# Performance work log

Hardware: AMD Instinct MI355X
Metric: run time of the kernel (lower is better)

The kernel has to match this reference:

```python
import jax, jax.numpy as jnp
import numpy as np

B, S, D, H = 4, 2048, 1024, 16
HD = D // H


def setup_inputs() -> dict:
    key = jax.random.key(0)
    ks = jax.random.split(key, 12)
    inp = {
        "query": jax.random.normal(ks[0], (B, S, D), jnp.float32),
        "key": jax.random.normal(ks[1], (B, S, D), jnp.float32),
        "value": jax.random.normal(ks[2], (B, S, D), jnp.float32),
        "mask": jnp.tril(jnp.ones((S, S), jnp.int32)),  # causal mask
        "Wq": jax.random.normal(ks[3], (D, D), jnp.float32) / np.sqrt(D),
        "bq": jax.random.normal(ks[4], (D,), jnp.float32) * 0.02,
        "Wk": jax.random.normal(ks[5], (D, D), jnp.float32) / np.sqrt(D),
        "bk": jax.random.normal(ks[6], (D,), jnp.float32) * 0.02,
        "Wv": jax.random.normal(ks[7], (D, D), jnp.float32) / np.sqrt(D),
        "bv": jax.random.normal(ks[8], (D,), jnp.float32) * 0.02,
        "Wo": jax.random.normal(ks[9], (D, D), jnp.float32) / np.sqrt(D),
        "bo": jax.random.normal(ks[10], (D,), jnp.float32) * 0.02,
    }
    return inp


def reference(query, key, value, mask, Wq, bq, Wk, bk, Wv, bv, Wo, bo):
    # Linear projections (torch nn.Linear: y = x @ W.T + b)
    q = query @ Wq.T + bq
    k = key @ Wk.T + bk
    v = value @ Wv.T + bv
    # split heads: [B, S, D] -> [B, H, S, HD]
    q = q.reshape(B, S, H, HD).transpose(0, 2, 1, 3)
    k = k.reshape(B, S, H, HD).transpose(0, 2, 1, 3)
    v = v.reshape(B, S, H, HD).transpose(0, 2, 1, 3)
    # scaled dot-product attention with full [B,H,S,S] scores (faithful to source)
    scores = jnp.einsum("bhqd,bhkd->bhqk", q, k) / jnp.sqrt(jnp.float32(HD))
    scores = jnp.where(mask == 0, -jnp.inf, scores)
    attn = jax.nn.softmax(scores, axis=-1)
    out = jnp.einsum("bhqk,bhkd->bhqd", attn, v)
    # merge heads and output projection (dropout rate = 0.0 -> identity)
    out = out.transpose(0, 2, 1, 3).reshape(B, S, D)
    return out @ Wo.T + bo
```

## Files before the change

### kernel.cpp

```cpp
#include <hip/hip_runtime.h>

typedef __bf16 bf16x8 __attribute__((ext_vector_type(8)));
typedef float f32x4 __attribute__((ext_vector_type(4)));
typedef float f32x16 __attribute__((ext_vector_type(16)));
typedef unsigned short ushort;

__device__ __forceinline__ int4 cvt8(float4 a, float4 b) {
  bf16x8 v;
  v[0] = (__bf16)a.x; v[1] = (__bf16)a.y; v[2] = (__bf16)a.z; v[3] = (__bf16)a.w;
  v[4] = (__bf16)b.x; v[5] = (__bf16)b.y; v[6] = (__bf16)b.z; v[7] = (__bf16)b.w;
  return __builtin_bit_cast(int4, v);
}

__device__ __forceinline__ void gld16(const void* g, void* l) {
  __builtin_amdgcn_global_load_lds(
      (const __attribute__((address_space(1))) void*)g,
      (__attribute__((address_space(3))) void*)l, 16, 0, 0);
}

__device__ __forceinline__ unsigned pkbf(float a, float b) {
  const unsigned x = __builtin_bit_cast(ushort, (__bf16)a);
  const unsigned y = __builtin_bit_cast(ushort, (__bf16)b);
  return x | (y << 16);
}

#if __has_builtin(__builtin_amdgcn_permlane32_swap)
typedef unsigned u32x2 __attribute__((ext_vector_type(2)));
__device__ __forceinline__ void plswap(unsigned& a, unsigned& b, int hi) {
  (void)hi;
  u32x2 r = __builtin_amdgcn_permlane32_swap(a, b, false, false);
  a = r[0]; b = r[1];
}
#else
__device__ __forceinline__ void plswap(unsigned& a, unsigned& b, int hi) {
  const unsigned pa = (unsigned)__shfl_xor((int)a, 32);
  const unsigned pb = (unsigned)__shfl_xor((int)b, 32);
  const unsigned x = hi ? pb : a;
  const unsigned y = hi ? b : pa;
  a = x; b = y;
}
#endif

__device__ __forceinline__ f32x16 mfma32(bf16x8 a, bf16x8 b, f32x16 c) {
  return __builtin_amdgcn_mfma_f32_32x32x16_bf16(a, b, c, 0, 0, 0);
}

__global__ __launch_bounds__(256) void cvt4_k(const float* __restrict__ i0,
                                              const float* __restrict__ i1,
                                              const float* __restrict__ i2,
                                              const float* __restrict__ i3,
                                              ushort* __restrict__ o, int n8) {
  const int z = blockIdx.y;
  const float* in = (z == 0) ? i0 : (z == 1) ? i1 : (z == 2) ? i2 : i3;
  ushort* out = o + (size_t)z * 1024 * 1024;
  int i = blockIdx.x * 256 + threadIdx.x;
  if (i >= n8) return;
  const float4* p = (const float4*)in + (size_t)i * 2;
  *(int4*)(out + (size_t)i * 8) = cvt8(p[0], p[1]);
}

template <int AMODE, int WMODE, int OMODE>
__global__ __launch_bounds__(256) void gemm_k(const void* __restrict__ A,
                                              const void* __restrict__ W,
                                              const float* __restrict__ bias,
                                              void* __restrict__ Out,
                                              float oscale) {
  constexpr int K = 1024;
  __shared__ __align__(16) char lA[128 * 128];
  __shared__ __align__(16) char lB[128 * 128];
  const int t = threadIdx.x;
  const int l = t & 63;
  const int w = t >> 6;
  const int wr = w >> 1, wc = w & 1;
  const int m0 = blockIdx.x * 128;
  const int n0 = blockIdx.y * 128;
  const int srow = l >> 3;
  const int scol = ((l & 7) ^ srow) << 3;
  f32x4 acc[4][4];
#pragma unroll
  for (int i = 0; i < 4; ++i)
#pragma unroll
    for (int j = 0; j < 4; ++j) acc[i][j] = (f32x4){0.f, 0.f, 0.f, 0.f};

  for (int k0 = 0; k0 < K; k0 += 64) {
    if constexpr (AMODE == 1) {
#pragma unroll
      for (int i = 0; i < 4; ++i) {
        const int chunk = w * 4 + i;
        gld16((const ushort*)A + (size_t)(m0 + chunk * 8 + srow) * K + k0 + scol,
              lA + chunk * 1024);
      }
    } else {
#pragma unroll
      for (int qq = 0; qq < 4; ++qq) {
        const int L = t * 8 + qq * 2048;
        const int r = L >> 6, c = L & 63;
        const int dst = r * 128 + ((c * 2) ^ ((r & 7) << 4));
        const float* s0 = (const float*)A + (size_t)(m0 + r) * K + k0 + c;
        *(int4*)(lA + dst) = cvt8(*(const float4*)s0, *(const float4*)(s0 + 4));
      }
    }
    if constexpr (WMODE == 1) {
#pragma unroll
      for (int i = 0; i < 4; ++i) {
        const int chunk = w * 4 + i;
        gld16((const ushort*)W + (size_t)(n0 + chunk * 8 + srow) * K + k0 + scol,
              lB + chunk * 1024);
      }
    } else {
#pragma unroll
      for (int qq = 0; qq < 4; ++qq) {
        const int L = t * 8 + qq * 2048;
        const int r = L >> 6, c = L & 63;
        const int dst = r * 128 + ((c * 2) ^ ((r & 7) << 4));
        const float* s1 = (const float*)W + (size_t)(n0 + r) * K + k0 + c;
        *(int4*)(lB + dst) = cvt8(*(const float4*)s1, *(const float4*)(s1 + 4));
      }
    }
    __syncthreads();
#pragma unroll
    for (int ks = 0; ks < 2; ++ks) {
      const int kb = ks * 64 + ((l >> 4) << 4);
      bf16x8 af[4], bfv[4];
#pragma unroll
      for (int i = 0; i < 4; ++i) {
        const int row = wr * 64 + i * 16 + (l & 15);
        af[i] = *(const bf16x8*)(lA + row * 128 + (kb ^ ((row & 7) << 4)));
      }
#pragma unroll
      for (int j = 0; j < 4; ++j) {
        const int row = wc * 64 + j * 16 + (l & 15);
        bfv[j] = *(const bf16x8*)(lB + row * 128 + (kb ^ ((row & 7) << 4)));
      }
#pragma unroll
      for (int i = 0; i < 4; ++i)
#pragma unroll
        for (int j = 0; j < 4; ++j)
          acc[i][j] = __builtin_amdgcn_mfma_f32_16x16x32_bf16(af[i], bfv[j],
                                                              acc[i][j], 0, 0, 0);
    }
    __syncthreads();
  }
#pragma unroll
  for (int i = 0; i < 4; ++i)
#pragma unroll
    for (int j = 0; j < 4; ++j)
#pragma unroll
      for (int rg = 0; rg < 4; ++rg) {
        const int gm = m0 + wr * 64 + i * 16 + ((l >> 4) << 2) + rg;
        const int gn = n0 + wc * 64 + j * 16 + (l & 15);
        const float v = (acc[i][j][rg] + bias[gn]) * oscale;
        if constexpr (OMODE == 0) {
          const int b = gm >> 11, s = gm & 2047, h = gn >> 6, hd = gn & 63;
          ((ushort*)Out)[((((size_t)(b * 16 + h)) * 2048 + s) << 6) + hd] =
              __builtin_bit_cast(ushort, (__bf16)v);
        } else if constexpr (OMODE == 1) {
          const int b = gm >> 11, s = gm & 2047, h = gn >> 6, hd = gn & 63;
          ((ushort*)Out)[((((size_t)(b * 16 + h)) << 6) + hd) * 2048 + s] =
              __builtin_bit_cast(ushort, (__bf16)v);
        } else {
          ((float*)Out)[(size_t)gm * 1024 + gn] = v;
        }
      }
}

__global__ __launch_bounds__(256) void attn_k(const ushort* __restrict__ qh,
                                              const ushort* __restrict__ kh,
                                              const ushort* __restrict__ vth,
                                              ushort* __restrict__ out) {
  const int bh = blockIdx.x;
  const int t = threadIdx.x, l = t & 63, wv = t >> 6;
  const int lq = l & 31, hi = l >> 5;
  __shared__ __align__(16) char lk[2][64 * 128];
  __shared__ __align__(16) char lv[2][64 * 128];

  const int r0 = t >> 3;
  const int c0 = (t & 7) * 8;
  const ushort* kbase = kh + (size_t)bh * 2048 * 64 + (size_t)r0 * 64 + c0;
  const ushort* vbase = vth + (size_t)bh * 64 * 2048 + (size_t)r0 * 2048 + c0;
  const int dst0 = r0 * 128 + ((c0 * 2) ^ ((r0 & 7) << 4));
  const int b = bh >> 4, h = bh & 15;

  int4 ka, kb2, va, vb2;
#define LOAD_TILE(kv0)                                            \
  do {                                                            \
    ka  = *(const int4*)(kbase + (size_t)(kv0) * 64);             \
    kb2 = *(const int4*)(kbase + (size_t)(kv0) * 64 + 32 * 64);   \
    va  = *(const int4*)(vbase + (kv0));                          \
    vb2 = *(const int4*)(vbase + (kv0) + 32 * 2048);              \
  } while (0)
#define WRITE_TILE(buf)                                           \
  do {                                                            \
    *(int4*)(lk[buf] + dst0) = ka;                                \
    *(int4*)(lk[buf] + dst0 + 32 * 128) = kb2;                    \
    *(int4*)(lv[buf] + dst0) = va;                                \
    *(int4*)(lv[buf] + dst0 + 32 * 128) = vb2;                    \
  } while (0)

#pragma unroll 1
  for (int pass = 0; pass < 2; ++pass) {
    const int qt = pass ? (15 - blockIdx.y) : blockIdx.y;
    const int q0 = qt * 128;
    const int qrow = q0 + wv * 32 + lq;

    bf16x8 qf0, qf1, qf2, qf3;
    {
      const ushort* qp = qh + ((size_t)bh * 2048 + qrow) * 64 + hi * 8;
      qf0 = *(const bf16x8*)(qp);
      qf1 = *(const bf16x8*)(qp + 16);
      qf2 = *(const bf16x8*)(qp + 32);
      qf3 = *(const bf16x8*)(qp + 48);
    }
    LOAD_TILE(0);
    __syncthreads();
    WRITE_TILE(0);

    float m_r = -1e30f, l_r = 0.f;
    f32x16 acco[2];
#pragma unroll
    for (int dt = 0; dt < 2; ++dt)
#pragma unroll
      for (int r = 0; r < 16; ++r) acco[dt][r] = 0.f;

    const int nt = 2 * qt + 2;
    int cur = 0;
#pragma unroll 1
    for (int ti = 0; ti < nt; ++ti) {
      __syncthreads();
      if (ti + 1 < nt) LOAD_TILE((ti + 1) << 6);

#pragma unroll
      for (int s = 0; s < 2; ++s) {
        const int kvs = (ti << 6) + s * 32;
        if (kvs > q0 + wv * 32 + 31) continue;

        f32x16 p;
#pragma unroll
        for (int r = 0; r < 16; ++r) p[r] = 0.f;
        __builtin_amdgcn_s_setprio(1);
#pragma unroll
        for (int kd = 0; kd < 4; ++kd) {
          const int row = s * 32 + lq;
          const bf16x8 kf = *(const bf16x8*)(
              lk[cur] + row * 128 + ((kd * 32 + hi * 16) ^ ((row & 7) << 4)));
          const bf16x8 qf = (kd == 0) ? qf0 : (kd == 1) ? qf1 : (kd == 2) ? qf2 : qf3;
          p = mfma32(kf, qf, p);
        }
        __builtin_amdgcn_s_setprio(0);
        if (kvs + 31 > q0 + wv * 32) {
#pragma unroll
          for (int r = 0; r < 16; ++r) {
            const int kv = kvs + (r & 3) + 8 * (r >> 2) + 4 * hi;
            if (kv > qrow) p[r] = -1e30f;
          }
        }
        float red[8];
#pragma unroll
        for (int r = 0; r < 8; ++r) red[r] = fmaxf(p[r], p[r + 8]);
#pragma unroll
        for (int r = 0; r < 4; ++r) red[r] = fmaxf(red[r], red[r + 4]);
        float tm = fmaxf(fmaxf(red[0], red[1]), fmaxf(red[2], red[3]));
        tm = fmaxf(tm, __shfl_xor(tm, 32));
        if (!__all(tm <= m_r + 8.f)) {
          const float mn = fmaxf(m_r, tm);
          const float e = __builtin_amdgcn_exp2f(m_r - mn);
          m_r = mn;
          l_r *= e;
#pragma unroll
          for (int dt = 0; dt < 2; ++dt)
#pragma unroll
            for (int r = 0; r < 16; ++r) acco[dt][r] *= e;
        }
#pragma unroll
        for (int r = 0; r < 16; ++r) p[r] = __builtin_amdgcn_exp2f(p[r] - m_r);
        float sr[8];
#pragma unroll
        for (int r = 0; r < 8; ++r) sr[r] = p[r] + p[r + 8];
#pragma unroll
        for (int r = 0; r < 4; ++r) sr[r] = sr[r] + sr[r + 4];
        float rs = (sr[0] + sr[1]) + (sr[2] + sr[3]);
        rs += __shfl_xor(rs, 32);
        l_r += rs;
        unsigned W0a = pkbf(p[0], p[1]),   W0b = pkbf(p[2], p[3]);
        unsigned W1a = pkbf(p[4], p[5]),   W1b = pkbf(p[6], p[7]);
        unsigned W2a = pkbf(p[8], p[9]),   W2b = pkbf(p[10], p[11]);
        unsigned W3a = pkbf(p[12], p[13]), W3b = pkbf(p[14], p[15]);
#pragma unroll
        for (int ks = 0; ks < 2; ++ks) {
          unsigned a0 = ks ? W2a : W0a;
          unsigned a1 = ks ? W2b : W0b;
          unsigned b0 = ks ? W3a : W1a;
          unsigned b1 = ks ? W3b : W1b;
          plswap(a0, b0, hi);
          plswap(a1, b1, hi);
          const uint4 pw = {a0, a1, b0, b1};
          const bf16x8 pf = __builtin_bit_cast(bf16x8, pw);
          __builtin_amdgcn_s_setprio(1);
#pragma unroll
          for (int dt = 0; dt < 2; ++dt) {
            const int row = dt * 32 + lq;
            const bf16x8 vf = *(const bf16x8*)(
                lv[cur] + row * 128 +
                ((s * 64 + ks * 32 + hi * 16) ^ ((row & 7) << 4)));
            acco[dt] = mfma32(vf, pf, acco[dt]);
          }
          __builtin_amdgcn_s_setprio(0);
        }
      }
      if (ti + 1 < nt) WRITE_TILE(cur ^ 1);
      cur ^= 1;
    }
    const float inv = __builtin_amdgcn_rcpf(l_r);
    ushort* orow = out + ((size_t)(b * 2048 + qrow)) * 1024 + h * 64;
#pragma unroll
    for (int dt = 0; dt < 2; ++dt)
#pragma unroll
      for (int g = 0; g < 4; ++g) {
        ushort4 st;
        st.x = __builtin_bit_cast(ushort, (__bf16)(acco[dt][4 * g + 0] * inv));
        st.y = __builtin_bit_cast(ushort, (__bf16)(acco[dt][4 * g + 1] * inv));
        st.z = __builtin_bit_cast(ushort, (__bf16)(acco[dt][4 * g + 2] * inv));
        st.w = __builtin_bit_cast(ushort, (__bf16)(acco[dt][4 * g + 3] * inv));
        *(ushort4*)(orow + dt * 32 + g * 8 + hi * 4) = st;
      }
  }
#undef LOAD_TILE
#undef WRITE_TILE
}

extern "C" void kernel_launch(void* const* d_in, const int* in_sizes, int n_in,
                              void* d_out, int out_size, void* d_ws, size_t ws_size,
                              hipStream_t stream) {
  (void)in_sizes; (void)n_in; (void)out_size;
  const float* query = (const float*)d_in[0];
  const float* key = (const float*)d_in[1];
  const float* value = (const float*)d_in[2];
  const float* Wq = (const float*)d_in[4];
  const float* bq = (const float*)d_in[5];
  const float* Wk = (const float*)d_in[6];
  const float* bk = (const float*)d_in[7];
  const float* Wv = (const float*)d_in[8];
  const float* bv = (const float*)d_in[9];
  const float* Wo = (const float*)d_in[10];
  const float* bo = (const float*)d_in[11];

  char* ws = (char*)d_ws;
  const size_t SZA = (size_t)8192 * 1024 * 2;
  const size_t SZW = (size_t)1024 * 1024 * 2;
  ushort* qh = (ushort*)(ws + 0 * SZA);
  ushort* kh = (ushort*)(ws + 1 * SZA);
  ushort* vt = (ushort*)(ws + 2 * SZA);
  ushort* ao = (ushort*)(ws + 3 * SZA);
  dim3 bb(256), gg(64, 8), ga(64, 8);
  const float QS = 0.125f * 1.44269504088896f;

  if (ws_size >= 4 * SZA + 4 * SZW) {
    ushort* wq = (ushort*)(ws + 4 * SZA);
    ushort* wk = (ushort*)(ws + 4 * SZA + 1 * SZW);
    ushort* wv = (ushort*)(ws + 4 * SZA + 2 * SZW);
    ushort* wo = (ushort*)(ws + 4 * SZA + 3 * SZW);
    const int n8w = 1024 * 1024 / 8;
    hipLaunchKernelGGL(cvt4_k, dim3(n8w / 256, 4), bb, 0, stream, Wq, Wk, Wv, Wo, wq, n8w);
    hipLaunchKernelGGL((gemm_k<0, 1, 0>), gg, bb, 0, stream, (const void*)query, (const void*)wq, bq, (void*)qh, QS);
    hipLaunchKernelGGL((gemm_k<0, 1, 0>), gg, bb, 0, stream, (const void*)key, (const void*)wk, bk, (void*)kh, 1.0f);
    hipLaunchKernelGGL((gemm_k<0, 1, 1>), gg, bb, 0, stream, (const void*)value, (const void*)wv, bv, (void*)vt, 1.0f);
    hipLaunchKernelGGL(attn_k, ga, bb, 0, stream, qh, kh, vt, ao);
    hipLaunchKernelGGL((gemm_k<1, 1, 2>), gg, bb, 0, stream, (const void*)ao, (const void*)wo, bo, d_out, 1.0f);
  } else {
    hipLaunchKernelGGL((gemm_k<0, 0, 0>), gg, bb, 0, stream, (const void*)query, (const void*)Wq, bq, (void*)qh, QS);
    hipLaunchKernelGGL((gemm_k<0, 0, 0>), gg, bb, 0, stream, (const void*)key, (const void*)Wk, bk, (void*)kh, 1.0f);
    hipLaunchKernelGGL((gemm_k<0, 0, 1>), gg, bb, 0, stream, (const void*)value, (const void*)Wv, bv, (void*)vt, 1.0f);
    hipLaunchKernelGGL(attn_k, ga, bb, 0, stream, qh, kh, vt, ao);
    hipLaunchKernelGGL((gemm_k<1, 0, 2>), gg, bb, 0, stream, (const void*)ao, (const void*)Wo, bo, d_out, 1.0f);
  }
}
```

Baseline: 206.8 us.

## Split paired causal query tiles into separate blocks and compute row sums via MFMA

The attention kernel stops processing two complementary query tiles per block. It launches one block per query tile, with twice as many blocks in y, ordered heaviest-first. The softmax row sum is now accumulated with an extra MFMA against a ones vector instead of VALU adds plus a cross-lane shuffle. The change also drops the s_setprio hints, reshapes the max reduction tree, and packs bf16 through a vector cast. This is meant to raise occupancy and parallelism and to cut VALU work, at the cost of losing the paired load balance and adding MFMA work and registers for the sum accumulator.

```diff
diff --git a/kernel.cpp b/kernel.cpp
--- a/kernel.cpp
+++ b/kernel.cpp
@@ -1,6 +1,7 @@
 #include <hip/hip_runtime.h>
 
 typedef __bf16 bf16x8 __attribute__((ext_vector_type(8)));
+typedef __bf16 bf16x2 __attribute__((ext_vector_type(2)));
 typedef float f32x4 __attribute__((ext_vector_type(4)));
 typedef float f32x16 __attribute__((ext_vector_type(16)));
 typedef unsigned short ushort;
@@ -19,9 +20,10 @@
 }
 
 __device__ __forceinline__ unsigned pkbf(float a, float b) {
-  const unsigned x = __builtin_bit_cast(ushort, (__bf16)a);
-  const unsigned y = __builtin_bit_cast(ushort, (__bf16)b);
-  return x | (y << 16);
+  bf16x2 v;
+  v[0] = (__bf16)a;
+  v[1] = (__bf16)b;
+  return __builtin_bit_cast(unsigned, v);
 }
 
 #if __has_builtin(__builtin_amdgcn_permlane32_swap)
@@ -169,17 +171,31 @@
                                               const ushort* __restrict__ vth,
                                               ushort* __restrict__ out) {
   const int bh = blockIdx.x;
+  const int qt = gridDim.y - 1 - blockIdx.y;
+  const int q0 = qt * 128;
   const int t = threadIdx.x, l = t & 63, wv = t >> 6;
   const int lq = l & 31, hi = l >> 5;
   __shared__ __align__(16) char lk[2][64 * 128];
   __shared__ __align__(16) char lv[2][64 * 128];
+
+  const int qrow = q0 + wv * 32 + lq;
+  bf16x8 qf0, qf1, qf2, qf3;
+  {
+    const ushort* qp = qh + ((size_t)bh * 2048 + qrow) * 64 + hi * 8;
+    qf0 = *(const bf16x8*)(qp);
+    qf1 = *(const bf16x8*)(qp + 16);
+    qf2 = *(const bf16x8*)(qp + 32);
+    qf3 = *(const bf16x8*)(qp + 48);
+  }
+  bf16x8 ones8;
+#pragma unroll
+  for (int i = 0; i < 8; ++i) ones8[i] = (__bf16)1.0f;
 
   const int r0 = t >> 3;
   const int c0 = (t & 7) * 8;
   const ushort* kbase = kh + (size_t)bh * 2048 * 64 + (size_t)r0 * 64 + c0;
   const ushort* vbase = vth + (size_t)bh * 64 * 2048 + (size_t)r0 * 2048 + c0;
   const int dst0 = r0 * 128 + ((c0 * 2) ^ ((r0 & 7) << 4));
-  const int b = bh >> 4, h = bh & 15;
 
   int4 ka, kb2, va, vb2;
 #define LOAD_TILE(kv0)                                            \
@@ -197,135 +213,115 @@
     *(int4*)(lv[buf] + dst0 + 32 * 128) = vb2;                    \
   } while (0)
 
+  LOAD_TILE(0);
+  WRITE_TILE(0);
+
+  float m_r = -1e30f;
+  f32x16 acco[2];
+  f32x16 acc_l;
+#pragma unroll
+  for (int dt = 0; dt < 2; ++dt)
+#pragma unroll
+    for (int r = 0; r < 16; ++r) acco[dt][r] = 0.f;
+#pragma unroll
+  for (int r = 0; r < 16; ++r) acc_l[r] = 0.f;
+
+  const int nt = 2 * qt + 2;
+  int cur = 0;
 #pragma unroll 1
-  for (int pass = 0; pass < 2; ++pass) {
-    const int qt = pass ? (15 - blockIdx.y) : blockIdx.y;
-    const int q0 = qt * 128;
-    const int qrow = q0 + wv * 32 + lq;
-
-    bf16x8 qf0, qf1, qf2, qf3;
-    {
-      const ushort* qp = qh + ((size_t)bh * 2048 + qrow) * 64 + hi * 8;
-      qf0 = *(const bf16x8*)(qp);
-      qf1 = *(const bf16x8*)(qp + 16);
-      qf2 = *(const bf16x8*)(qp + 32);
-      qf3 = *(const bf16x8*)(qp + 48);
-    }
-    LOAD_TILE(0);
+  for (int ti = 0; ti < nt; ++ti) {
     __syncthreads();
-    WRITE_TILE(0);
-
-    float m_r = -1e30f, l_r = 0.f;
-    f32x16 acco[2];
-#pragma unroll
-    for (int dt = 0; dt < 2; ++dt)
-#pragma unroll
-      for (int r = 0; r < 16; ++r) acco[dt][r] = 0.f;
-
-    const int nt = 2 * qt + 2;
-    int cur = 0;
-#pragma unroll 1
-    for (int ti = 0; ti < nt; ++ti) {
-      __syncthreads();
-      if (ti + 1 < nt) LOAD_TILE((ti + 1) << 6);
-
-#pragma unroll
-      for (int s = 0; s < 2; ++s) {
-        const int kvs = (ti << 6) + s * 32;
-        if (kvs > q0 + wv * 32 + 31) continue;
-
-        f32x16 p;
-#pragma unroll
-        for (int r = 0; r < 16; ++r) p[r] = 0.f;
-        __builtin_amdgcn_s_setprio(1);
-#pragma unroll
-        for (int kd = 0; kd < 4; ++kd) {
-          const int row = s * 32 + lq;
-          const bf16x8 kf = *(const bf16x8*)(
-              lk[cur] + row * 128 + ((kd * 32 + hi * 16) ^ ((row & 7) << 4)));
-          const bf16x8 qf = (kd == 0) ? qf0 : (kd == 1) ? qf1 : (kd == 2) ? qf2 : qf3;
-          p = mfma32(kf, qf, p);
+    if (ti + 1 < nt) LOAD_TILE((ti + 1) << 6);
+
+#pragma unroll
+    for (int s = 0; s < 2; ++s) {
+      const int kvs = (ti << 6) + s * 32;
+      if (kvs > q0 + wv * 32 + 31) continue;
+
+      f32x16 p;
+#pragma unroll
+      for (int r = 0; r < 16; ++r) p[r] = 0.f;
+#pragma unroll
+      for (int kd = 0; kd < 4; ++kd) {
+        const int row = s * 32 + lq;
+        const bf16x8 kf = *(const bf16x8*)(
+            lk[cur] + row * 128 + ((kd * 32 + hi * 16) ^ ((row & 7) << 4)));
+        const bf16x8 qf = (kd == 0) ? qf0 : (kd == 1) ? qf1 : (kd == 2) ? qf2 : qf3;
+        p = mfma32(kf, qf, p);
+      }
+      if (kvs + 31 > q0 + wv * 32) {
+#pragma unroll
+        for (int r = 0; r < 16; ++r) {
+          const int kv = kvs + (r & 3) + 8 * (r >> 2) + 4 * hi;
+          if (kv > qrow) p[r] = -1e30f;
         }
-        __builtin_amdgcn_s_setprio(0);
-        if (kvs + 31 > q0 + wv * 32) {
-#pragma unroll
-          for (int r = 0; r < 16; ++r) {
-            const int kv = kvs + (r & 3) + 8 * (r >> 2) + 4 * hi;
-            if (kv > qrow) p[r] = -1e30f;
-          }
+      }
+      const float a0 = fmaxf(fmaxf(p[0], p[1]), p[2]);
+      const float a1 = fmaxf(fmaxf(p[3], p[4]), p[5]);
+      const float a2 = fmaxf(fmaxf(p[6], p[7]), p[8]);
+      const float a3 = fmaxf(fmaxf(p[9], p[10]), p[11]);
+      const float a4 = fmaxf(fmaxf(p[12], p[13]), p[14]);
+      const float b0 = fmaxf(fmaxf(a0, a1), a2);
+      const float b1 = fmaxf(fmaxf(a3, a4), p[15]);
+      float tm = fmaxf(b0, b1);
+      tm = fmaxf(tm, __shfl_xor(tm, 32));
+      if (!__all(tm <= m_r + 8.f)) {
+        const float mn = fmaxf(m_r, tm);
+        const float e = __builtin_amdgcn_exp2f(m_r - mn);
+        m_r = mn;
+#pragma unroll
+        for (int dt = 0; dt < 2; ++dt)
+#pragma unroll
+          for (int r = 0; r < 16; ++r) acco[dt][r] *= e;
+#pragma unroll
+        for (int r = 0; r < 16; ++r) acc_l[r] *= e;
+      }
+#pragma unroll
+      for (int r = 0; r < 16; ++r) p[r] = __builtin_amdgcn_exp2f(p[r] - m_r);
+      unsigned W0a = pkbf(p[0], p[1]),   W0b = pkbf(p[2], p[3]);
+      unsigned W1a = pkbf(p[4], p[5]),   W1b = pkbf(p[6], p[7]);
+      unsigned W2a = pkbf(p[8], p[9]),   W2b = pkbf(p[10], p[11]);
+      unsigned W3a = pkbf(p[12], p[13]), W3b = pkbf(p[14], p[15]);
+#pragma unroll
+      for (int ks = 0; ks < 2; ++ks) {
+        unsigned a0u = ks ? W2a : W0a;
+        unsigned a1u = ks ? W2b : W0b;
+        unsigned b0u = ks ? W3a : W1a;
+        unsigned b1u = ks ? W3b : W1b;
+        plswap(a0u, b0u, hi);
+        plswap(a1u, b1u, hi);
+        const uint4 pw = {a0u, a1u, b0u, b1u};
+        const bf16x8 pf = __builtin_bit_cast(bf16x8, pw);
+        acc_l = mfma32(ones8, pf, acc_l);
+#pragma unroll
+        for (int dt = 0; dt < 2; ++dt) {
+          const int row = dt * 32 + lq;
+          const bf16x8 vf = *(const bf16x8*)(
+              lv[cur] + row * 128 +
+              ((s * 64 + ks * 32 + hi * 16) ^ ((row & 7) << 4)));
+          acco[dt] = mfma32(vf, pf, acco[dt]);
         }
-        float red[8];
-#pragma unroll
-        for (int r = 0; r < 8; ++r) red[r] = fmaxf(p[r], p[r + 8]);
-#pragma unroll
-        for (int r = 0; r < 4; ++r) red[r] = fmaxf(red[r], red[r + 4]);
-        float tm = fmaxf(fmaxf(red[0], red[1]), fmaxf(red[2], red[3]));
-        tm = fmaxf(tm, __shfl_xor(tm, 32));
-        if (!__all(tm <= m_r + 8.f)) {
-          const float mn = fmaxf(m_r, tm);
-          const float e = __builtin_amdgcn_exp2f(m_r - mn);
-          m_r = mn;
-          l_r *= e;
-#pragma unroll
-          for (int dt = 0; dt < 2; ++dt)
-#pragma unroll
-            for (int r = 0; r < 16; ++r) acco[dt][r] *= e;
-        }
-#pragma unroll
-        for (int r = 0; r < 16; ++r) p[r] = __builtin_amdgcn_exp2f(p[r] - m_r);
-        float sr[8];
-#pragma unroll
-        for (int r = 0; r < 8; ++r) sr[r] = p[r] + p[r + 8];
-#pragma unroll
-        for (int r = 0; r < 4; ++r) sr[r] = sr[r] + sr[r + 4];
-        float rs = (sr[0] + sr[1]) + (sr[2] + sr[3]);
-        rs += __shfl_xor(rs, 32);
-        l_r += rs;
-        unsigned W0a = pkbf(p[0], p[1]),   W0b = pkbf(p[2], p[3]);
-        unsigned W1a = pkbf(p[4], p[5]),   W1b = pkbf(p[6], p[7]);
-        unsigned W2a = pkbf(p[8], p[9]),   W2b = pkbf(p[10], p[11]);
-        unsigned W3a = pkbf(p[12], p[13]), W3b = pkbf(p[14], p[15]);
-#pragma unroll
-        for (int ks = 0; ks < 2; ++ks) {
-          unsigned a0 = ks ? W2a : W0a;
-          unsigned a1 = ks ? W2b : W0b;
-          unsigned b0 = ks ? W3a : W1a;
-          unsigned b1 = ks ? W3b : W1b;
-          plswap(a0, b0, hi);
-          plswap(a1, b1, hi);
-          const uint4 pw = {a0, a1, b0, b1};
-          const bf16x8 pf = __builtin_bit_cast(bf16x8, pw);
-          __builtin_amdgcn_s_setprio(1);
-#pragma unroll
-          for (int dt = 0; dt < 2; ++dt) {
-            const int row = dt * 32 + lq;
-            const bf16x8 vf = *(const bf16x8*)(
-                lv[cur] + row * 128 +
-                ((s * 64 + ks * 32 + hi * 16) ^ ((row & 7) << 4)));
-            acco[dt] = mfma32(vf, pf, acco[dt]);
-          }
-          __builtin_amdgcn_s_setprio(0);
-        }
-      }
-      if (ti + 1 < nt) WRITE_TILE(cur ^ 1);
-      cur ^= 1;
-    }
-    const float inv = __builtin_amdgcn_rcpf(l_r);
-    ushort* orow = out + ((size_t)(b * 2048 + qrow)) * 1024 + h * 64;
-#pragma unroll
-    for (int dt = 0; dt < 2; ++dt)
-#pragma unroll
-      for (int g = 0; g < 4; ++g) {
-        ushort4 st;
-        st.x = __builtin_bit_cast(ushort, (__bf16)(acco[dt][4 * g + 0] * inv));
-        st.y = __builtin_bit_cast(ushort, (__bf16)(acco[dt][4 * g + 1] * inv));
-        st.z = __builtin_bit_cast(ushort, (__bf16)(acco[dt][4 * g + 2] * inv));
-        st.w = __builtin_bit_cast(ushort, (__bf16)(acco[dt][4 * g + 3] * inv));
-        *(ushort4*)(orow + dt * 32 + g * 8 + hi * 4) = st;
-      }
+      }
+    }
+    if (ti + 1 < nt) WRITE_TILE(cur ^ 1);
+    cur ^= 1;
   }
 #undef LOAD_TILE
 #undef WRITE_TILE
+  const int b = bh >> 4, h = bh & 15;
+  const float inv = __builtin_amdgcn_rcpf(acc_l[0]);
+  ushort* orow = out + ((size_t)(b * 2048 + qrow)) * 1024 + h * 64;
+#pragma unroll
+  for (int dt = 0; dt < 2; ++dt)
+#pragma unroll
+    for (int g = 0; g < 4; ++g) {
+      ushort4 st;
+      st.x = __builtin_bit_cast(ushort, (__bf16)(acco[dt][4 * g + 0] * inv));
+      st.y = __builtin_bit_cast(ushort, (__bf16)(acco[dt][4 * g + 1] * inv));
+      st.z = __builtin_bit_cast(ushort, (__bf16)(acco[dt][4 * g + 2] * inv));
+      st.w = __builtin_bit_cast(ushort, (__bf16)(acco[dt][4 * g + 3] * inv));
+      *(ushort4*)(orow + dt * 32 + g * 8 + hi * 4) = st;
+    }
 }
 
 extern "C" void kernel_launch(void* const* d_in, const int* in_sizes, int n_in,
@@ -351,7 +347,7 @@
   ushort* kh = (ushort*)(ws + 1 * SZA);
   ushort* vt = (ushort*)(ws + 2 * SZA);
   ushort* ao = (ushort*)(ws + 3 * SZA);
-  dim3 bb(256), gg(64, 8), ga(64, 8);
+  dim3 bb(256), gg(64, 8), ga(64, 16);
   const float QS = 0.125f * 1.44269504088896f;
 
   if (ws_size >= 4 * SZA + 4 * SZW) {
```

After: 198.6 us. 1.04x faster.
